# Performance work log

Hardware: AMD Instinct MI355X
Metric: run time of the kernel (lower is better)

Reference implementation:

```python
import jax, jax.numpy as jnp
import numpy as np

B, S = 32, 4096          # decode batch, kv cache length
HID, H = 5120, 16        # hidden size, local heads
DN, DR, DV = 128, 64, 128  # qk_nope, qk_rope, v head dims
QL, KL = 1536, 512       # q_lora_rank, kv_lora_rank
BASE = 10000.0
EPS = 1e-6
SCALE = (DN + DR) ** -0.5


def rmsnorm(x, w):
    return x * jax.lax.rsqrt(jnp.mean(x * x, axis=-1, keepdims=True) + EPS) * w


def rope_interleaved(x, pos):
    # non-neox (interleaved pairs) rope, per-row positions pos: [B]
    d = x.shape[-1]
    inv = 1.0 / (BASE ** (jnp.arange(0, d, 2, dtype=jnp.float32) / d))  # [d/2]
    fr = pos.astype(jnp.float32)[:, None] * inv                          # [B, d/2]
    cos, sin = jnp.cos(fr), jnp.sin(fr)
    x1, x2 = x[..., 0::2], x[..., 1::2]
    while cos.ndim < x1.ndim:  # broadcast over head dim if present
        cos, sin = cos[:, None], sin[:, None]
    o1 = x1 * cos - x2 * sin
    o2 = x2 * cos + x1 * sin
    return jnp.stack([o1, o2], axis=-1).reshape(x.shape)


def setup_inputs() -> dict:
    key = jax.random.key(0)
    ks = jax.random.split(key, 9)
    w = 0.02  # weight scale for sane activations
    return {
        "hidden_states": jax.random.normal(ks[0], (B, HID), jnp.float32),
        "positions": jax.random.randint(ks[1], (B,), 0, S, jnp.int32),
        "kv_cache_latent": jax.random.normal(ks[2], (B, S, KL), jnp.float32),
        "kv_cache_rope": jax.random.normal(ks[3], (B, S, DR), jnp.float32),
        "w_qkv_a": jax.random.normal(ks[4], (HID, QL + KL + DR), jnp.float32) * w,
        "q_a_norm_w": jnp.ones((QL,), jnp.float32),
        "w_q_b": jax.random.normal(ks[5], (QL, H * (DN + DR)), jnp.float32) * w,
        "kv_a_norm_w": jnp.ones((KL,), jnp.float32),
        "w_kc": jax.random.normal(ks[6], (H, DN, KL), jnp.float32) * w,
        "w_vc": jax.random.normal(ks[7], (H, KL, DV), jnp.float32) * w,
        "w_o": jax.random.normal(ks[8], (H * DV, HID), jnp.float32) * w,
    }


def reference(hidden_states, positions, kv_cache_latent, kv_cache_rope,
              w_qkv_a, q_a_norm_w, w_q_b, kv_a_norm_w, w_kc, w_vc, w_o):
    # fused qkv_a projection -> q_lora | kv latent | k_pe
    qkv = hidden_states @ w_qkv_a                       # [B, QL+KL+DR]
    q_a, latent, k_pe = jnp.split(qkv, [QL, QL + KL], axis=-1)

    # q path: rmsnorm -> q_b_proj -> per-head split nope/pe
    q = (rmsnorm(q_a, q_a_norm_w) @ w_q_b).reshape(B, H, DN + DR)
    q_nope, q_pe = q[..., :DN], q[..., DN:]
    q_pe = rope_interleaved(q_pe, positions)            # [B, H, DR]

    # kv latent path: rmsnorm latent, rope k_pe, write current token into cache
    latent_n = rmsnorm(latent, kv_a_norm_w)             # [B, KL]
    k_pe = rope_interleaved(k_pe, positions)            # [B, DR]
    cache_l = kv_cache_latent.at[:, -1, :].set(latent_n)  # [B, S, KL]
    cache_r = kv_cache_rope.at[:, -1, :].set(k_pe)        # [B, S, DR]

    # weight absorption: q_nope absorbed through w_kc into latent space
    q_abs = jnp.einsum("bhd,hdc->bhc", q_nope, w_kc)    # [B, H, KL]

    # MQA attention over latent KV (1 kv head shared by all q heads)
    scores = (jnp.einsum("bhc,bsc->bhs", q_abs, cache_l)
              + jnp.einsum("bhr,bsr->bhs", q_pe, cache_r)) * SCALE
    attn = jax.nn.softmax(scores, axis=-1)              # [B, H, S]
    ctx = jnp.einsum("bhs,bsc->bhc", attn, cache_l)     # [B, H, KL]

    # un-absorb values through w_vc, then output projection
    out = jnp.einsum("bhc,hcv->bhv", ctx, w_vc).reshape(B, H * DV)
    return out @ w_o                                    # [B, HID]
```

## Files before the change

kernel.cpp:

```cpp
#include <hip/hip_runtime.h>
#include <hip/hip_bf16.h>
#include <stdint.h>

#define B_   32
#define S_   4096
#define HID_ 5120
#define H_   16
#define DN_  128
#define DR_  64
#define DV_  128
#define QL_  1536
#define KL_  512
#define KC_  576
#define NQKV_ 2112
#define NQB_  3072
#define EPS_ 1e-6f
#define SCALE_ 0.07216878364870323f

typedef __attribute__((ext_vector_type(4))) float f32x4;
typedef __attribute__((ext_vector_type(8))) short s16x8;
typedef __attribute__((ext_vector_type(2))) unsigned int u32x2;
typedef __attribute__((ext_vector_type(4))) unsigned int u32x4;

__device__ __forceinline__ unsigned short bf(float f) {
  union { __hip_bfloat16 h; unsigned short u; } v;
  v.h = __float2bfloat16(f);
  return v.u;
}
__device__ __forceinline__ unsigned int bf2(float x, float y) {
  union { __hip_bfloat162 h; unsigned int u; } v;
  v.h = __float22bfloat162_rn(float2{x, y});
  return v.u;
}
__device__ __forceinline__ s16x8 pack8(const float* w) {
  union { u32x4 q; s16x8 s; } v;
  v.q = (u32x4){bf2(w[0], w[1]), bf2(w[2], w[3]), bf2(w[4], w[5]), bf2(w[6], w[7])};
  return v.s;
}

template<int K, int TK, int N>
__global__ __launch_bounds__(256) void gemm_bf(const unsigned short* __restrict__ Abf,
                                               const float* __restrict__ W,
                                               float* __restrict__ P) {
  int t = threadIdx.x, wave = t >> 6, lane = t & 63;
  int quad = lane >> 4, lo = lane & 15;
  int n0 = blockIdx.x * 64 + wave * 16;
  int k0 = blockIdx.y * TK;
  f32x4 acc0 = {0.f, 0.f, 0.f, 0.f}, acc1 = {0.f, 0.f, 0.f, 0.f};
  const float* wp = W + (size_t)(k0 + quad * 8) * N + n0 + lo;
  const unsigned short* a0p = Abf + (size_t)lo * K + k0 + quad * 8;
  const unsigned short* a1p = Abf + (size_t)(16 + lo) * K + k0 + quad * 8;
#pragma unroll 2
  for (int kk = 0; kk < TK / 32; ++kk) {
    s16x8 a0 = *(const s16x8*)(a0p + kk * 32);
    s16x8 a1 = *(const s16x8*)(a1p + kk * 32);
    float wv[8];
#pragma unroll
    for (int j = 0; j < 8; ++j) wv[j] = wp[((size_t)kk * 32 + j) * N];
    s16x8 bfv = pack8(wv);
    acc0 = __builtin_amdgcn_mfma_f32_16x16x32_bf16(a0, bfv, acc0, 0, 0, 0);
    acc1 = __builtin_amdgcn_mfma_f32_16x16x32_bf16(a1, bfv, acc1, 0, 0, 0);
  }
  float* p = P + ((size_t)blockIdx.y * B_) * N + n0 + lo;
#pragma unroll
  for (int reg = 0; reg < 4; ++reg) {
    p[(size_t)(quad * 4 + reg) * N]      = acc0[reg];
    p[(size_t)(16 + quad * 4 + reg) * N] = acc1[reg];
  }
}

template<int K, int TK, int N>
__global__ __launch_bounds__(256) void gemm_f32a(const float* __restrict__ A,
                                                 const float* __restrict__ W,
                                                 float* __restrict__ P) {
  int t = threadIdx.x, wave = t >> 6, lane = t & 63;
  int quad = lane >> 4, lo = lane & 15;
  int n0 = blockIdx.x * 64 + wave * 16;
  int k0 = blockIdx.y * TK;
  f32x4 acc0 = {0.f, 0.f, 0.f, 0.f}, acc1 = {0.f, 0.f, 0.f, 0.f};
  const float* wp = W + (size_t)(k0 + quad * 8) * N + n0 + lo;
  const float* a0p = A + (size_t)lo * K + k0 + quad * 8;
  const float* a1p = A + (size_t)(16 + lo) * K + k0 + quad * 8;
#pragma unroll 2
  for (int kk = 0; kk < TK / 32; ++kk) {
    f32x4 x0 = *(const f32x4*)(a0p + kk * 32);
    f32x4 x1 = *(const f32x4*)(a0p + kk * 32 + 4);
    f32x4 y0 = *(const f32x4*)(a1p + kk * 32);
    f32x4 y1 = *(const f32x4*)(a1p + kk * 32 + 4);
    float a0f[8], a1f[8];
#pragma unroll
    for (int j = 0; j < 4; ++j) {
      a0f[j] = x0[j]; a0f[4 + j] = x1[j];
      a1f[j] = y0[j]; a1f[4 + j] = y1[j];
    }
    s16x8 a0 = pack8(a0f);
    s16x8 a1 = pack8(a1f);
    float wv[8];
#pragma unroll
    for (int j = 0; j < 8; ++j) wv[j] = wp[((size_t)kk * 32 + j) * N];
    s16x8 bfv = pack8(wv);
    acc0 = __builtin_amdgcn_mfma_f32_16x16x32_bf16(a0, bfv, acc0, 0, 0, 0);
    acc1 = __builtin_amdgcn_mfma_f32_16x16x32_bf16(a1, bfv, acc1, 0, 0, 0);
  }
  float* p = P + ((size_t)blockIdx.y * B_) * N + n0 + lo;
#pragma unroll
  for (int reg = 0; reg < 4; ++reg) {
    p[(size_t)(quad * 4 + reg) * N]      = acc0[reg];
    p[(size_t)(16 + quad * 4 + reg) * N] = acc1[reg];
  }
}

#define NSL1 32
#define NSL2 24
#define NSL3 16

__global__ __launch_bounds__(256) void k2a(const float* __restrict__ P1, const float* __restrict__ qw,
                    const float* __restrict__ kvw, const int* __restrict__ pos,
                    unsigned short* __restrict__ qn_bf, float* __restrict__ latent_n,
                    float* __restrict__ kpe_rot, float* __restrict__ cs_buf) {
  int b = blockIdx.y, t = threadIdx.x;
  __shared__ float row[QL_];
  __shared__ float red[256];
  if (blockIdx.x == 0) {
    float sq = 0.f;
    for (int n = t; n < QL_; n += 256) {
      float s = 0.f;
#pragma unroll
      for (int ks = 0; ks < NSL1; ++ks) s += P1[((size_t)ks * B_ + b) * NQKV_ + n];
      row[n] = s; sq += s * s;
    }
    red[t] = sq;
    __syncthreads();
    for (int off = 128; off > 0; off >>= 1) {
      if (t < off) red[t] += red[t + off];
      __syncthreads();
    }
    float rq = 1.0f / sqrtf(red[0] / QL_ + EPS_);
    for (int n = t; n < QL_; n += 256) qn_bf[(size_t)b * QL_ + n] = bf(row[n] * rq * qw[n]);
  } else {
    float sl = 0.f;
    for (int n = t; n < KL_ + DR_; n += 256) {
      float s = 0.f;
#pragma unroll
      for (int ks = 0; ks < NSL1; ++ks) s += P1[((size_t)ks * B_ + b) * NQKV_ + QL_ + n];
      row[n] = s;
      if (n < KL_) sl += s * s;
    }
    red[t] = sl;
    __syncthreads();
    for (int off = 128; off > 0; off >>= 1) {
      if (t < off) red[t] += red[t + off];
      __syncthreads();
    }
    float rl = 1.0f / sqrtf(red[0] / KL_ + EPS_);
    for (int n = t; n < KL_; n += 256) latent_n[(size_t)b * KL_ + n] = row[n] * rl * kvw[n];
    if (t < 32) {
      double inv = exp(-((double)t / 32.0) * log(10000.0));
      float fr = (float)pos[b] * (float)inv;
      float c = (float)cos((double)fr), s = (float)sin((double)fr);
      cs_buf[(b * 32 + t) * 2] = c; cs_buf[(b * 32 + t) * 2 + 1] = s;
      float x1 = row[KL_ + 2 * t], x2 = row[KL_ + 2 * t + 1];
      kpe_rot[b * DR_ + 2 * t]     = x1 * c - x2 * s;
      kpe_rot[b * DR_ + 2 * t + 1] = x2 * c + x1 * s;
    }
  }
}

__global__ __launch_bounds__(256) void k2c(const float* __restrict__ P2,
                                           const float* __restrict__ w_kc,
                                           const float* __restrict__ cs_buf,
                                           unsigned short* __restrict__ q_cat) {
  int b = blockIdx.y, t = threadIdx.x, wave = t >> 6, lane = t & 63;
  int hl = blockIdx.x * 2;
  __shared__ float qh[2][192];
  for (int j = t; j < 384; j += 256) {
    int hh = j / 192, jj = j - hh * 192;
    float s = 0.f;
    int col = (hl + hh) * 192 + jj;
#pragma unroll
    for (int ks = 0; ks < NSL2; ++ks) s += P2[((size_t)ks * B_ + b) * NQB_ + col];
    qh[hh][jj] = s;
  }
  __syncthreads();
  if (t < 64) {
    int hh = t >> 5, ll = t & 31;
    float c = cs_buf[(b * 32 + ll) * 2], s = cs_buf[(b * 32 + ll) * 2 + 1];
    float x1 = qh[hh][DN_ + 2 * ll], x2 = qh[hh][DN_ + 2 * ll + 1];
    qh[hh][DN_ + 2 * ll]     = x1 * c - x2 * s;
    qh[hh][DN_ + 2 * ll + 1] = x2 * c + x1 * s;
  }
  __syncthreads();
  int hh = wave >> 1, half = wave & 1;
  int h = hl + hh;
  float acc[4] = {0.f, 0.f, 0.f, 0.f};
  const float* wk = w_kc + (size_t)h * DN_ * KL_ + half * 256;
#pragma unroll 2
  for (int d = 0; d < DN_; ++d) {
    float qd = qh[hh][d];
#pragma unroll
    for (int i = 0; i < 4; ++i)
      acc[i] = fmaf(qd, wk[(size_t)d * KL_ + lane + 64 * i], acc[i]);
  }
  unsigned short* qc = q_cat + ((size_t)b * H_ + h) * KC_;
#pragma unroll
  for (int i = 0; i < 4; ++i) qc[half * 256 + lane + 64 * i] = bf(acc[i] * SCALE_);
  if (half == 0) qc[KL_ + lane] = bf(qh[hh][DN_ + lane] * SCALE_);
}

#define LP_ 584
#define CHUNK_ 256
#define TR_ 32
#define NTL_ 8

__global__ __launch_bounds__(256, 2) void attn(
    const float* __restrict__ cache_l, const float* __restrict__ cache_r,
    const float* __restrict__ latent_n, const float* __restrict__ kpe_rot,
    const unsigned short* __restrict__ q_cat,
    float* __restrict__ ws_acc, float* __restrict__ ws_ml) {
  int chunk = blockIdx.x, b = blockIdx.y;
  int t = threadIdx.x, wave = t >> 6, lane = t & 63;
  int quad = lane >> 4, lo = lane & 15;

  __shared__ __attribute__((aligned(16))) unsigned short Lt[TR_ * LP_];
  __shared__ __attribute__((aligned(16))) unsigned short pb[4][H_ * TR_];

  s16x8 af[18];
  const unsigned short* qc = q_cat + ((size_t)b * H_ + lo) * KC_;
#pragma unroll
  for (int ks = 0; ks < 18; ++ks) af[ks] = *(const s16x8*)(qc + ks * 32 + quad * 8);

  f32x4 accc[NTL_];
#pragma unroll
  for (int i = 0; i < NTL_; ++i) accc[i] = (f32x4){0.f, 0.f, 0.f, 0.f};
  float m_run[4], l_run[4];
#pragma unroll
  for (int r = 0; r < 4; ++r) { m_run[r] = -3.0e38f; l_run[r] = 0.f; }

  int r8 = t >> 3, u = t & 7;

  float4 v[18];
  auto load_tile = [&](int tile) {
    int s = chunk * CHUNK_ + tile * TR_ + r8;
    const float* rl = cache_l + ((size_t)b * S_ + s) * KL_;
    const float* rr = cache_r + ((size_t)b * S_ + s) * DR_;
    if (s == S_ - 1) { rl = latent_n + (size_t)b * KL_; rr = kpe_rot + (size_t)b * DR_; }
#pragma unroll
    for (int j = 0; j < 18; ++j) {
      int c = u * 4 + j * 32;
      v[j] = *(const float4*)((j < 16) ? (rl + c) : (rr + (c - 512)));
    }
  };
  load_tile(0);

#pragma unroll 1
  for (int tile = 0; tile < NTL_; ++tile) {
    __syncthreads();
#pragma unroll
    for (int j = 0; j < 18; ++j) {
      int c = u * 4 + j * 32;
      u32x2 o; o[0] = bf2(v[j].x, v[j].y); o[1] = bf2(v[j].z, v[j].w);
      *(u32x2*)(&Lt[r8 * LP_ + c]) = o;
    }
    if (tile + 1 < NTL_) load_tile(tile + 1);
    __syncthreads();
    f32x4 sc0 = {0.f, 0.f, 0.f, 0.f}, sc1 = {0.f, 0.f, 0.f, 0.f};
#pragma unroll
    for (int ks = 0; ks < 18; ++ks) {
      s16x8 b0 = *(const s16x8*)(&Lt[lo * LP_ + ks * 32 + quad * 8]);
      s16x8 b1 = *(const s16x8*)(&Lt[(16 + lo) * LP_ + ks * 32 + quad * 8]);
      sc0 = __builtin_amdgcn_mfma_f32_16x16x32_bf16(af[ks], b0, sc0, 0, 0, 0);
      sc1 = __builtin_amdgcn_mfma_f32_16x16x32_bf16(af[ks], b1, sc1, 0, 0, 0);
    }
#pragma unroll
    for (int reg = 0; reg < 4; ++reg) {
      float s0 = sc0[reg], s1 = sc1[reg];
      float mt = fmaxf(s0, s1);
#pragma unroll
      for (int m = 1; m < 16; m <<= 1) mt = fmaxf(mt, __shfl_xor(mt, m, 64));
      float mn = fmaxf(m_run[reg], mt);
      float alpha = __expf(m_run[reg] - mn);
      m_run[reg] = mn;
      float p0 = __expf(s0 - mn), p1 = __expf(s1 - mn);
      float lt = p0 + p1;
#pragma unroll
      for (int m = 1; m < 16; m <<= 1) lt += __shfl_xor(lt, m, 64);
      l_run[reg] = l_run[reg] * alpha + lt;
#pragma unroll
      for (int i = 0; i < NTL_; ++i) accc[i][reg] *= alpha;
      int h = quad * 4 + reg;
      pb[wave][h * TR_ + lo]      = bf(p0);
      pb[wave][h * TR_ + 16 + lo] = bf(p1);
    }
    s16x8 ap = *(const s16x8*)(&pb[wave][lo * TR_ + quad * 8]);
#pragma unroll
    for (int nt = 0; nt < NTL_; ++nt) {
      int c = wave * 128 + nt * 16 + lo;
      s16x8 bv;
#pragma unroll
      for (int j = 0; j < 8; ++j) bv[j] = (short)Lt[(quad * 8 + j) * LP_ + c];
      accc[nt] = __builtin_amdgcn_mfma_f32_16x16x32_bf16(ap, bv, accc[nt], 0, 0, 0);
    }
  }
  float* accp = ws_acc + (((size_t)b * 16 + chunk) * H_) * KL_;
#pragma unroll
  for (int nt = 0; nt < NTL_; ++nt) {
    int c = wave * 128 + nt * 16 + lo;
#pragma unroll
    for (int reg = 0; reg < 4; ++reg)
      accp[(size_t)(quad * 4 + reg) * KL_ + c] = accc[nt][reg];
  }
  if (wave == 0 && lo == 0) {
#pragma unroll
    for (int reg = 0; reg < 4; ++reg) {
      int h = quad * 4 + reg;
      ws_ml[(((size_t)b * 16 + chunk) * H_ + h) * 2 + 0] = m_run[reg];
      ws_ml[(((size_t)b * 16 + chunk) * H_ + h) * 2 + 1] = l_run[reg];
    }
  }
}

__global__ __launch_bounds__(256) void combine(const float* __restrict__ ws_acc,
                        const float* __restrict__ ws_ml,
                        const float* __restrict__ w_vc, unsigned short* __restrict__ o_v) {
  int h = blockIdx.x, b = blockIdx.y, t = threadIdx.x;
  __shared__ float sm[16], sl[16];
  __shared__ float ctx[KL_];
  __shared__ float ps[256];
  if (t < 16) {
    sm[t] = ws_ml[(((size_t)b * 16 + t) * H_ + h) * 2];
    sl[t] = ws_ml[(((size_t)b * 16 + t) * H_ + h) * 2 + 1];
  }
  __syncthreads();
  float M = -3e38f;
#pragma unroll
  for (int i = 0; i < 16; ++i) M = fmaxf(M, sm[i]);
  float wkk[16]; float Lsum = 0.f;
#pragma unroll
  for (int i = 0; i < 16; ++i) { wkk[i] = __expf(sm[i] - M); Lsum += wkk[i] * sl[i]; }
  float invL = 1.0f / Lsum;
  for (int c = t; c < KL_; c += 256) {
    float s = 0.f;
#pragma unroll
    for (int i = 0; i < 16; ++i)
      s += wkk[i] * ws_acc[(((size_t)b * 16 + i) * H_ + h) * KL_ + c];
    ctx[c] = s * invL;
  }
  __syncthreads();
  int vv = t & 127, half = t >> 7;
  const float* wv = w_vc + (size_t)h * KL_ * DV_;
  float s0 = 0.f, s1 = 0.f;
#pragma unroll 4
  for (int k = half * 256; k < half * 256 + 256; k += 2) {
    s0 = fmaf(ctx[k],     wv[(size_t)k * DV_ + vv],       s0);
    s1 = fmaf(ctx[k + 1], wv[(size_t)(k + 1) * DV_ + vv], s1);
  }
  ps[t] = s0 + s1;
  __syncthreads();
  if (t < 128) o_v[(size_t)b * (H_ * DV_) + h * DV_ + t] = bf(ps[t] + ps[t + 128]);
}

__global__ __launch_bounds__(256) void reduce_out(const float* __restrict__ P, float* __restrict__ out) {
  int i = blockIdx.x * 256 + threadIdx.x;
  const f32x4* P4 = (const f32x4*)P;
  f32x4 s = P4[i];
#pragma unroll
  for (int ks = 1; ks < NSL3; ++ks) s += P4[(size_t)ks * 40960 + i];
  ((f32x4*)out)[i] = s;
}

extern "C" void kernel_launch(void* const* d_in, const int* in_sizes, int n_in,
                              void* d_out, int out_size, void* d_ws, size_t ws_size,
                              hipStream_t stream) {
  const float* hs    = (const float*)d_in[0];
  const int*   pos   = (const int*)d_in[1];
  const float* cl    = (const float*)d_in[2];
  const float* cr    = (const float*)d_in[3];
  const float* w_qkv = (const float*)d_in[4];
  const float* qnw   = (const float*)d_in[5];
  const float* w_qb  = (const float*)d_in[6];
  const float* kvnw  = (const float*)d_in[7];
  const float* w_kc  = (const float*)d_in[8];
  const float* w_vc  = (const float*)d_in[9];
  const float* w_o   = (const float*)d_in[10];
  float* out = (float*)d_out;

  char* ws = (char*)d_ws;
  float* ws_acc = (float*)(ws);
  float* P1     = (float*)(ws + 16777216);
  float* P2     = (float*)(ws + 25427968);
  float* P5     = (float*)(ws + 34865152);
  unsigned short* qn_bf = (unsigned short*)(ws + 45350912);
  float* latent_n = (float*)(ws + 45449216);
  float* kpe_rot  = (float*)(ws + 45514752);
  float* cs_buf   = (float*)(ws + 45522944);
  unsigned short* q_cat = (unsigned short*)(ws + 45531136);
  float* ws_ml    = (float*)(ws + 46120960);
  unsigned short* o_v_bf = (unsigned short*)(ws + 46186496);

  gemm_f32a<HID_, 160, NQKV_><<<dim3(33, 32), 256, 0, stream>>>(hs, w_qkv, P1);
  k2a<<<dim3(2, 32), 256, 0, stream>>>(P1, qnw, kvnw, pos, qn_bf, latent_n, kpe_rot, cs_buf);
  gemm_bf<QL_, 64, NQB_><<<dim3(48, 24), 256, 0, stream>>>(qn_bf, w_qb, P2);
  k2c<<<dim3(8, 32), 256, 0, stream>>>(P2, w_kc, cs_buf, q_cat);
  attn<<<dim3(16, 32), 256, 0, stream>>>(cl, cr, latent_n, kpe_rot, q_cat, ws_acc, ws_ml);
  combine<<<dim3(16, 32), 256, 0, stream>>>(ws_acc, ws_ml, w_vc, o_v_bf);
  gemm_bf<H_ * DV_, 128, HID_><<<dim3(80, 16), 256, 0, stream>>>(o_v_bf, w_o, P5);
  reduce_out<<<160, 256, 0, stream>>>(P5, out);
}
```

Baseline: 551.3 us.

## Retile attention LDS layout and use ds_read_b64_tr_b16 for PV operand

```diff
diff --git a/kernel.cpp b/kernel.cpp
--- a/kernel.cpp
+++ b/kernel.cpp
@@ -36,6 +36,12 @@
   union { u32x4 q; s16x8 s; } v;
   v.q = (u32x4){bf2(w[0], w[1]), bf2(w[2], w[3]), bf2(w[4], w[5]), bf2(w[6], w[7])};
   return v.s;
+}
+
+__device__ __forceinline__ u32x2 ds_tr16(unsigned addr) {
+  u32x2 d;
+  asm volatile("ds_read_b64_tr_b16 %0, %1" : "=v"(d) : "v"(addr));
+  return d;
 }
 
 template<int K, int TK, int N>
@@ -207,10 +213,10 @@
   if (half == 0) qc[KL_ + lane] = bf(qh[hh][DN_ + lane] * SCALE_);
 }
 
-#define LP_ 584
 #define CHUNK_ 256
 #define TR_ 32
 #define NTL_ 8
+#define NSUB_ 36
 
 __global__ __launch_bounds__(256, 2) void attn(
     const float* __restrict__ cache_l, const float* __restrict__ cache_r,
@@ -221,7 +227,7 @@
   int t = threadIdx.x, wave = t >> 6, lane = t & 63;
   int quad = lane >> 4, lo = lane & 15;
 
-  __shared__ __attribute__((aligned(16))) unsigned short Lt[TR_ * LP_];
+  __shared__ __attribute__((aligned(16))) unsigned short Lt[8 * NSUB_ * 64];
   __shared__ __attribute__((aligned(16))) unsigned short pb[4][H_ * TR_];
 
   s16x8 af[18];
@@ -238,7 +244,7 @@
 
   int r8 = t >> 3, u = t & 7;
 
-  float4 v[18];
+  u32x2 o[18];
   auto load_tile = [&](int tile) {
     int s = chunk * CHUNK_ + tile * TR_ + r8;
     const float* rl = cache_l + ((size_t)b * S_ + s) * KL_;
@@ -247,10 +253,13 @@
 #pragma unroll
     for (int j = 0; j < 18; ++j) {
       int c = u * 4 + j * 32;
-      v[j] = *(const float4*)((j < 16) ? (rl + c) : (rr + (c - 512)));
+      float4 v = *(const float4*)((j < 16) ? (rl + c) : (rr + (c - 512)));
+      o[j][0] = bf2(v.x, v.y); o[j][1] = bf2(v.z, v.w);
     }
   };
   load_tile(0);
+
+  unsigned ltb = (unsigned)(size_t)(&Lt[0]);
 
 #pragma unroll 1
   for (int tile = 0; tile < NTL_; ++tile) {
@@ -258,19 +267,22 @@
 #pragma unroll
     for (int j = 0; j < 18; ++j) {
       int c = u * 4 + j * 32;
-      u32x2 o; o[0] = bf2(v[j].x, v[j].y); o[1] = bf2(v[j].z, v[j].w);
-      *(u32x2*)(&Lt[r8 * LP_ + c]) = o;
+      int e = ((r8 >> 2) * NSUB_ + (c >> 4)) * 64 + (r8 & 3) * 16 + (c & 15);
+      *(u32x2*)(&Lt[e]) = o[j];
     }
     if (tile + 1 < NTL_) load_tile(tile + 1);
     __syncthreads();
+
     f32x4 sc0 = {0.f, 0.f, 0.f, 0.f}, sc1 = {0.f, 0.f, 0.f, 0.f};
 #pragma unroll
     for (int ks = 0; ks < 18; ++ks) {
-      s16x8 b0 = *(const s16x8*)(&Lt[lo * LP_ + ks * 32 + quad * 8]);
-      s16x8 b1 = *(const s16x8*)(&Lt[(16 + lo) * LP_ + ks * 32 + quad * 8]);
+      int e0 = ((lo >> 2) * NSUB_ + 2 * ks + (quad >> 1)) * 64 + (lo & 3) * 16 + 8 * (quad & 1);
+      s16x8 b0 = *(const s16x8*)(&Lt[e0]);
+      s16x8 b1 = *(const s16x8*)(&Lt[e0 + 4 * NSUB_ * 64]);
       sc0 = __builtin_amdgcn_mfma_f32_16x16x32_bf16(af[ks], b0, sc0, 0, 0, 0);
       sc1 = __builtin_amdgcn_mfma_f32_16x16x32_bf16(af[ks], b1, sc1, 0, 0, 0);
     }
+
 #pragma unroll
     for (int reg = 0; reg < 4; ++reg) {
       float s0 = sc0[reg], s1 = sc1[reg];
@@ -292,15 +304,24 @@
       pb[wave][h * TR_ + 16 + lo] = bf(p1);
     }
     s16x8 ap = *(const s16x8*)(&pb[wave][lo * TR_ + quad * 8]);
+
+    u32x2 r0[NTL_], r1[NTL_];
 #pragma unroll
     for (int nt = 0; nt < NTL_; ++nt) {
-      int c = wave * 128 + nt * 16 + lo;
-      s16x8 bv;
-#pragma unroll
-      for (int j = 0; j < 8; ++j) bv[j] = (short)Lt[(quad * 8 + j) * LP_ + c];
-      accc[nt] = __builtin_amdgcn_mfma_f32_16x16x32_bf16(ap, bv, accc[nt], 0, 0, 0);
-    }
-  }
+      unsigned base = ltb + (unsigned)((((quad * 2) * NSUB_ + wave * 8 + nt) * 64) * 2 + lo * 8);
+      r0[nt] = ds_tr16(base);
+      r1[nt] = ds_tr16(base + NSUB_ * 128);
+    }
+    asm volatile("s_waitcnt lgkmcnt(0)" ::: "memory");
+    __builtin_amdgcn_sched_barrier(0);
+#pragma unroll
+    for (int nt = 0; nt < NTL_; ++nt) {
+      union { u32x2 d[2]; s16x8 s; } bb;
+      bb.d[0] = r0[nt]; bb.d[1] = r1[nt];
+      accc[nt] = __builtin_amdgcn_mfma_f32_16x16x32_bf16(ap, bb.s, accc[nt], 0, 0, 0);
+    }
+  }
+
   float* accp = ws_acc + (((size_t)b * 16 + chunk) * H_) * KL_;
 #pragma unroll
   for (int nt = 0; nt < NTL_; ++nt) {
```

Result: no change. 551.8 us (+0.1%).
